# Kernel tuning notes

Measured on AMD Instinct MI355X. Metric: run time of the kernel, lower is better.

The kernel has to match this reference:

```python
import jax, jax.numpy as jnp
import numpy as np

# ---- GLIFR / network constants (from RSNNNetwork.__init__ with defaults) ----
DT = 0.05
TAU = 5.0
KM = 1.0 / TAU          # k_m = 1/tau
R = 1.0 / 9.43
KSYN = 1.0
SPIKE_R = 20.0
SIGMA_V = 10.0
AVG = 5.0               # scalar mean of `target` (fixed constant here)
THRESH = float(SIGMA_V * np.log((SPIKE_R - AVG) / AVG))
ASC_AMP = np.array([-9.18, -198.94], np.float32)
ASC_R = np.array([1.0, 1.0], np.float32)
ASC_K = np.array([0.003, 0.1], np.float32)
DSDT = 0.9


def _wt(n_post):
    # weight-init center from RSNNNetwork.__init__
    wt = TAU / R * (SIGMA_V / DT) * (DSDT / n_post ** 2)
    wt = wt * (1.0 / (AVG * (1.0 - AVG / SPIKE_R))) / 1000.0
    return float(wt)


def setup_inputs() -> dict:
    key = jax.random.key(0)
    k1, k2, k3 = jax.random.split(key, 3)
    T, B, N0, N1 = 1000, 32, 256, 512
    inputs = jax.random.uniform(k1, (T, B, 1, N0), dtype=jnp.float32)
    wt = _wt(N1)
    W1 = jax.random.uniform(k2, (N1, N0), dtype=jnp.float32, minval=wt - 1.0, maxval=wt + 1.0)
    Wr = jax.random.uniform(k3, (N1, N1), dtype=jnp.float32, minval=wt - 1.0, maxval=wt + 1.0)
    return {"inputs": inputs, "W1": W1, "Wr": Wr}


_AK = jnp.asarray(ASC_K).reshape(2, 1, 1, 1)
_AA = jnp.asarray(ASC_AMP).reshape(2, 1, 1, 1)
_AR = jnp.asarray(ASC_R).reshape(2, 1, 1, 1)


def _glif_step(state, x):
    """Rate-based GLIF (GLIFR) update. state = (V, ascs, Isyn, delay_buf).
    V:[B,1,N], ascs:[2,B,1,N], Isyn:[B,1,N], buf:[delay,B,1,N].
    Returns (new_state, delayed_output, spikes)."""
    V, ascs, Isyn, buf = state
    Isyn = Isyn * (1.0 - DT * KSYN) + DT * KSYN * x          # synaptic current
    V = V * (1.0 - DT * KM) + DT * KM * R * (Isyn + ascs.sum(0))
    S = SPIKE_R * jax.nn.sigmoid((V - THRESH) / SIGMA_V)      # continuous firing rate
    ascs = ascs * (1.0 - DT * _AK) + _AA * _AR * S * DT        # after-spike currents
    out = buf[0]                                               # delay = 1 step
    buf = jnp.concatenate([buf[1:], S[None]], axis=0)
    return (V, ascs, Isyn, buf), out, S


def _zero_state(B, n):
    return (jnp.zeros((B, 1, n), jnp.float32),
            jnp.zeros((2, B, 1, n), jnp.float32),
            jnp.zeros((B, 1, n), jnp.float32),
            jnp.zeros((1, B, 1, n), jnp.float32))


def reference(inputs, W1, Wr):
    T, B = inputs.shape[0], inputs.shape[1]
    N0, N1 = inputs.shape[-1], W1.shape[0]

    def step(carry, x_t):
        s0, s1 = carry
        # input-layer GLIF (no linear)
        s0, o0, _ = _glif_step(s0, x_t)
        # feedforward linear -> glif1 (first call this step)
        h1 = jnp.einsum('bin,mn->bim', o0, W1)
        s1, o1, sp_a = _glif_step(s1, h1)
        # recurrent linear -> SAME glif1 again (second call this step)
        h2 = jnp.einsum('bin,mn->bim', o1, Wr)
        s1, _, sp_b = _glif_step(s1, h2)
        return (s0, s1), jnp.stack([sp_a, sp_b], axis=0)

    init = (_zero_state(B, N0), _zero_state(B, N1))
    _, spikes = jax.lax.scan(step, init, inputs)  # [T, 2, B, 1, N1]
    # spikes_all of the last GLIF: two appends per timestep, interleaved in call order
    return spikes.reshape(T * 2, B, 1, N1)
```

## Files before the change

### kernel.cpp

```cpp
#include <hip/hip_runtime.h>


#define T_STEPS 1000
#define NB 32
#define N0 256
#define N1 512

#define C_SYN_D 0.95f
#define C_SYN_I 0.05f
#define C_V_D   0.99f
#define C_KMR   0.0010604453870625663f
#define C_TH    10.986122886681098f
#define C_A0_D  0.99985f
#define C_A0_I  (-0.459f)
#define C_A1_D  0.995f
#define C_A1_I  (-9.947f)

__device__ __forceinline__ float glif_S(float V) {
  return 20.0f / (1.0f + __expf((C_TH - V) * 0.1f));
}

__global__ __launch_bounds__(64)
void layer0_scan(const float* __restrict__ x, float* __restrict__ S0) {
  const int g = blockIdx.x * 64 + threadIdx.x;
  float V = 0.f, a0 = 0.f, a1 = 0.f, Is = 0.f;
  float xb[8];
#pragma unroll
  for (int i = 0; i < 8; ++i) xb[i] = x[i * (NB * N0) + g];
#pragma unroll 1
  for (int tb = 0; tb < T_STEPS / 8; ++tb) {
#pragma unroll
    for (int u = 0; u < 8; ++u) {
      const int t = tb * 8 + u;
      const float xi = xb[u];
      const int tf = t + 8;
      if (tf < T_STEPS) xb[u] = x[tf * (NB * N0) + g];
      Is = fmaf(Is, C_SYN_D, C_SYN_I * xi);
      V  = fmaf(V, C_V_D, C_KMR * (Is + a0 + a1));
      const float S = glif_S(V);
      a0 = fmaf(a0, C_A0_D, C_A0_I * S);
      a1 = fmaf(a1, C_A1_D, C_A1_I * S);
      S0[t * (NB * N0) + g] = S;
    }
  }
}

__global__ __launch_bounds__(256, 1)
void rsnn_recur(const float* __restrict__ W1, const float* __restrict__ Wr,
                const float* __restrict__ S0, float* __restrict__ out,
                unsigned long long* __restrict__ xch) {
  const int wg  = blockIdx.x;
  const int b   = wg >> 3;
  const int s   = wg & 7;
  const int tid = threadIdx.x;
  const int mg  = tid >> 4;
  const int kc  = tid & 15;
  const int mBase = s * 64 + mg * 4;

  __shared__ float actS[16 * 36];
  __shared__ float actO[16 * 20];

  float4 wr4[4][8];
  float4 w14[4][4];
#pragma unroll
  for (int i = 0; i < 4; ++i) {
    const float4* rw = (const float4*)(Wr + (size_t)(mBase + i) * N1 + kc * 32);
#pragma unroll
    for (int j = 0; j < 8; ++j) wr4[i][j] = rw[j];
    const float4* r1 = (const float4*)(W1 + (size_t)(mBase + i) * N0 + kc * 16);
#pragma unroll
    for (int j = 0; j < 4; ++j) w14[i][j] = r1[j];
  }

  float V[4]   = {0.f, 0.f, 0.f, 0.f};
  float A0v[4] = {0.f, 0.f, 0.f, 0.f};
  float A1v[4] = {0.f, 0.f, 0.f, 0.f};
  float Is[4]  = {0.f, 0.f, 0.f, 0.f};

  bool gave_up = false;

#pragma unroll 1
  for (int t = 0; t < T_STEPS; ++t) {
    if (t == 0) {
      actS[(tid >> 5) * 36 + (tid & 31)] = 0.f;
      {
        const int k = tid + 256;
        actS[(k >> 5) * 36 + (k & 31)] = 0.f;
      }
      actO[(tid >> 4) * 20 + (tid & 15)] = 0.f;
    } else {
      const float v2 = S0[(size_t)(t - 1) * (NB * N0) + b * N0 + tid];
      const unsigned long long* px =
          xch + (size_t)((t - 1) & 1) * (NB * N1) + (size_t)b * N1;
      const unsigned tg = (unsigned)t;
      unsigned long long w0 = 0ull, w1 = 0ull;
      bool r0 = false, r1 = false;
      int iter = gave_up ? (1 << 30) : 0;
      for (;;) {
        if (!r0) {
          w0 = __hip_atomic_load(px + tid, __ATOMIC_RELAXED,
                                 __HIP_MEMORY_SCOPE_AGENT);
          r0 = ((unsigned)(w0 >> 32) == tg);
        }
        if (!r1) {
          w1 = __hip_atomic_load(px + tid + 256, __ATOMIC_RELAXED,
                                 __HIP_MEMORY_SCOPE_AGENT);
          r1 = ((unsigned)(w1 >> 32) == tg);
        }
        if (r0 && r1) break;
        if (++iter > (1 << 17)) { gave_up = true; break; }
        __builtin_amdgcn_s_sleep(1);
      }
      actS[(tid >> 5) * 36 + (tid & 31)] = __uint_as_float((unsigned)w0);
      {
        const int k = tid + 256;
        actS[(k >> 5) * 36 + (k & 31)] = __uint_as_float((unsigned)w1);
      }
      actO[(tid >> 4) * 20 + (tid & 15)] = v2;
    }
    __syncthreads();

    float h2a[4] = {0.f, 0.f, 0.f, 0.f};
    float h1a[4] = {0.f, 0.f, 0.f, 0.f};
    const float4* aS4 = (const float4*)actS;
    const float4* aO4 = (const float4*)actO;
#pragma unroll
    for (int j = 0; j < 8; ++j) {
      const float4 a = aS4[kc * 9 + j];
#pragma unroll
      for (int i = 0; i < 4; ++i) {
        h2a[i] = fmaf(wr4[i][j].x, a.x, h2a[i]);
        h2a[i] = fmaf(wr4[i][j].y, a.y, h2a[i]);
        h2a[i] = fmaf(wr4[i][j].z, a.z, h2a[i]);
        h2a[i] = fmaf(wr4[i][j].w, a.w, h2a[i]);
      }
    }
#pragma unroll
    for (int j = 0; j < 4; ++j) {
      const float4 a = aO4[kc * 5 + j];
#pragma unroll
      for (int i = 0; i < 4; ++i) {
        h1a[i] = fmaf(w14[i][j].x, a.x, h1a[i]);
        h1a[i] = fmaf(w14[i][j].y, a.y, h1a[i]);
        h1a[i] = fmaf(w14[i][j].z, a.z, h1a[i]);
        h1a[i] = fmaf(w14[i][j].w, a.w, h1a[i]);
      }
    }
    __syncthreads();

#pragma unroll
    for (int mask = 1; mask <= 8; mask <<= 1) {
#pragma unroll
      for (int i = 0; i < 4; ++i) {
        h2a[i] += __shfl_xor(h2a[i], mask, 64);
        h1a[i] += __shfl_xor(h1a[i], mask, 64);
      }
    }

    if (kc == 0) {
      float spa[4], spb[4];
#pragma unroll
      for (int i = 0; i < 4; ++i) {
        Is[i] = fmaf(Is[i], C_SYN_D, C_SYN_I * h1a[i]);
        V[i]  = fmaf(V[i], C_V_D, C_KMR * (Is[i] + A0v[i] + A1v[i]));
        const float Sa = glif_S(V[i]);
        A0v[i] = fmaf(A0v[i], C_A0_D, C_A0_I * Sa);
        A1v[i] = fmaf(A1v[i], C_A1_D, C_A1_I * Sa);
        spa[i] = Sa;
        Is[i] = fmaf(Is[i], C_SYN_D, C_SYN_I * h2a[i]);
        V[i]  = fmaf(V[i], C_V_D, C_KMR * (Is[i] + A0v[i] + A1v[i]));
        const float Sb = glif_S(V[i]);
        A0v[i] = fmaf(A0v[i], C_A0_D, C_A0_I * Sb);
        A1v[i] = fmaf(A1v[i], C_A1_D, C_A1_I * Sb);
        spb[i] = Sb;
      }
      float* outA = out + ((size_t)(2 * t) * NB + b) * N1 + mBase;
      *(float4*)outA = make_float4(spa[0], spa[1], spa[2], spa[3]);
      float* outB = out + ((size_t)(2 * t + 1) * NB + b) * N1 + mBase;
      *(float4*)outB = make_float4(spb[0], spb[1], spb[2], spb[3]);

      unsigned long long* qx =
          xch + (size_t)(t & 1) * (NB * N1) + (size_t)b * N1 + mBase;
      const unsigned long long tg1 = ((unsigned long long)(t + 1)) << 32;
#pragma unroll
      for (int i = 0; i < 4; ++i)
        __hip_atomic_store(qx + i,
                           tg1 | (unsigned long long)__float_as_uint(spb[i]),
                           __ATOMIC_RELAXED, __HIP_MEMORY_SCOPE_AGENT);
    }
  }
}

extern "C" void kernel_launch(void* const* d_in, const int* in_sizes, int n_in,
                              void* d_out, int out_size, void* d_ws, size_t ws_size,
                              hipStream_t stream) {
  const float* inputs = (const float*)d_in[0];
  const float* W1     = (const float*)d_in[1];
  const float* Wr     = (const float*)d_in[2];
  float* out = (float*)d_out;

  float* S0 = (float*)d_ws;
  unsigned long long* xch = (unsigned long long*)((char*)d_ws +
                              (size_t)T_STEPS * NB * N0 * sizeof(float));

  hipLaunchKernelGGL(layer0_scan, dim3((NB * N0) / 64), dim3(64), 0, stream,
                     inputs, S0);
  hipLaunchKernelGGL(rsnn_recur, dim3(256), dim3(256), 0, stream,
                     W1, Wr, S0, out, xch);
}
```

Before: 3.126 ms.

## Use XCD-local sc0 flag exchange with agent-scope fallback and remap blocks

Remaps block IDs so that all 8 slices of a batch row land on the same XCD, assuming round-robin block dispatch across the 8 XCDs. The inter-workgroup spike exchange then uses sc0 loads and stores, which stay within the XCD-local L2, instead of agent-scope atomics. This is meant to cut the latency of each per-timestep handshake. Every value is also written to a second agent-scope buffer, and a poller switches to that buffer if the fast path has not seen the value after a cap. This guards against the XCD-placement assumption failing, at the cost of duplicate stores.

```diff
diff --git a/kernel.cpp b/kernel.cpp
--- a/kernel.cpp
+++ b/kernel.cpp
@@ -5,6 +5,9 @@
 #define NB 32
 #define N0 256
 #define N1 512
+
+#define FAST_CAP 4096
+#define HARD_CAP (1 << 17)
 
 #define C_SYN_D 0.95f
 #define C_SYN_I 0.05f
@@ -48,10 +51,11 @@
 __global__ __launch_bounds__(256, 1)
 void rsnn_recur(const float* __restrict__ W1, const float* __restrict__ Wr,
                 const float* __restrict__ S0, float* __restrict__ out,
-                unsigned long long* __restrict__ xch) {
-  const int wg  = blockIdx.x;
-  const int b   = wg >> 3;
-  const int s   = wg & 7;
+                unsigned long long* __restrict__ xf,
+                unsigned long long* __restrict__ xs) {
+  const int bid = blockIdx.x;
+  const int b   = (bid & 7) * 4 + (bid >> 6);
+  const int s   = (bid >> 3) & 7;
   const int tid = threadIdx.x;
   const int mg  = tid >> 4;
   const int kc  = tid & 15;
@@ -78,6 +82,7 @@
   float Is[4]  = {0.f, 0.f, 0.f, 0.f};
 
   bool gave_up = false;
+  bool slow0 = false, slow1 = false;
 
 #pragma unroll 1
   for (int t = 0; t < T_STEPS; ++t) {
@@ -90,25 +95,43 @@
       actO[(tid >> 4) * 20 + (tid & 15)] = 0.f;
     } else {
       const float v2 = S0[(size_t)(t - 1) * (NB * N0) + b * N0 + tid];
-      const unsigned long long* px =
-          xch + (size_t)((t - 1) & 1) * (NB * N1) + (size_t)b * N1;
+      const size_t xoff = (size_t)((t - 1) & 1) * (NB * N1) + (size_t)b * N1;
+      const unsigned long long af =
+          (unsigned long long)(uintptr_t)(xf + xoff + tid);
+      const unsigned long long* ps = xs + xoff;
       const unsigned tg = (unsigned)t;
       unsigned long long w0 = 0ull, w1 = 0ull;
       bool r0 = false, r1 = false;
-      int iter = gave_up ? (1 << 30) : 0;
+      int iter = gave_up ? (HARD_CAP + 1) : 0;
       for (;;) {
         if (!r0) {
-          w0 = __hip_atomic_load(px + tid, __ATOMIC_RELAXED,
-                                 __HIP_MEMORY_SCOPE_AGENT);
-          r0 = ((unsigned)(w0 >> 32) == tg);
+          if (!slow0) {
+            asm volatile("global_load_dwordx2 %0, %1, off sc0"
+                         : "=v"(w0) : "v"(af) : "memory");
+          } else {
+            w0 = __hip_atomic_load(ps + tid, __ATOMIC_RELAXED,
+                                   __HIP_MEMORY_SCOPE_AGENT);
+          }
         }
         if (!r1) {
-          w1 = __hip_atomic_load(px + tid + 256, __ATOMIC_RELAXED,
-                                 __HIP_MEMORY_SCOPE_AGENT);
-          r1 = ((unsigned)(w1 >> 32) == tg);
+          if (!slow1) {
+            asm volatile("global_load_dwordx2 %0, %1, off offset:2048 sc0"
+                         : "=v"(w1) : "v"(af) : "memory");
+          } else {
+            w1 = __hip_atomic_load(ps + tid + 256, __ATOMIC_RELAXED,
+                                   __HIP_MEMORY_SCOPE_AGENT);
+          }
         }
+        asm volatile("s_waitcnt vmcnt(0)" ::: "memory");
+        if (!r0) r0 = ((unsigned)(w0 >> 32) == tg);
+        if (!r1) r1 = ((unsigned)(w1 >> 32) == tg);
         if (r0 && r1) break;
-        if (++iter > (1 << 17)) { gave_up = true; break; }
+        ++iter;
+        if (iter == FAST_CAP) {
+          slow0 = slow0 || !r0;
+          slow1 = slow1 || !r1;
+        }
+        if (iter > HARD_CAP) { gave_up = true; break; }
         __builtin_amdgcn_s_sleep(1);
       }
       actS[(tid >> 5) * 36 + (tid & 31)] = __uint_as_float((unsigned)w0);
@@ -179,14 +202,26 @@
       float* outB = out + ((size_t)(2 * t + 1) * NB + b) * N1 + mBase;
       *(float4*)outB = make_float4(spb[0], spb[1], spb[2], spb[3]);
 
-      unsigned long long* qx =
-          xch + (size_t)(t & 1) * (NB * N1) + (size_t)b * N1 + mBase;
+      const size_t qoff = (size_t)(t & 1) * (NB * N1) + (size_t)b * N1 + mBase;
       const unsigned long long tg1 = ((unsigned long long)(t + 1)) << 32;
+      unsigned long long tw[4];
 #pragma unroll
       for (int i = 0; i < 4; ++i)
-        __hip_atomic_store(qx + i,
-                           tg1 | (unsigned long long)__float_as_uint(spb[i]),
-                           __ATOMIC_RELAXED, __HIP_MEMORY_SCOPE_AGENT);
+        tw[i] = tg1 | (unsigned long long)__float_as_uint(spb[i]);
+      const unsigned long long qa =
+          (unsigned long long)(uintptr_t)(xf + qoff);
+      asm volatile("global_store_dwordx2 %0, %1, off sc0"
+                   :: "v"(qa), "v"(tw[0]) : "memory");
+      asm volatile("global_store_dwordx2 %0, %1, off offset:8 sc0"
+                   :: "v"(qa), "v"(tw[1]) : "memory");
+      asm volatile("global_store_dwordx2 %0, %1, off offset:16 sc0"
+                   :: "v"(qa), "v"(tw[2]) : "memory");
+      asm volatile("global_store_dwordx2 %0, %1, off offset:24 sc0"
+                   :: "v"(qa), "v"(tw[3]) : "memory");
+#pragma unroll
+      for (int i = 0; i < 4; ++i)
+        __hip_atomic_store(xs + qoff + i, tw[i], __ATOMIC_RELAXED,
+                           __HIP_MEMORY_SCOPE_AGENT);
     }
   }
 }
@@ -200,11 +235,12 @@
   float* out = (float*)d_out;
 
   float* S0 = (float*)d_ws;
-  unsigned long long* xch = (unsigned long long*)((char*)d_ws +
+  unsigned long long* xf = (unsigned long long*)((char*)d_ws +
                               (size_t)T_STEPS * NB * N0 * sizeof(float));
+  unsigned long long* xs = xf + (size_t)2 * NB * N1;
 
   hipLaunchKernelGGL(layer0_scan, dim3((NB * N0) / 64), dim3(64), 0, stream,
                      inputs, S0);
   hipLaunchKernelGGL(rsnn_recur, dim3(256), dim3(256), 0, stream,
-                     W1, Wr, S0, out, xch);
-}
+                     W1, Wr, S0, out, xf, xs);
+}
```

After: 10.65 ms. 241% more time.
